# Kernel optimization log

Measured on AMD Instinct MI355X. Metric: run time of the kernel, lower is better.

Reference implementation:

```python
import jax, jax.numpy as jnp
import numpy as np

EPS = 1e-6

def _rmsnorm(x, w):
    var = jnp.mean(x * x, axis=-1, keepdims=True)
    return x * jax.lax.rsqrt(var + EPS) * w

def _act_quant(x):
    # per-token int8 absmax quantization (BitNet b1.58)
    scale = 127.0 / jnp.clip(jnp.max(jnp.abs(x), axis=-1, keepdims=True), 1e-5)
    return jnp.round(jnp.clip(x * scale, -128.0, 127.0)) / scale

def _weight_quant(w):
    # per-tensor ternary quantization with mean-abs scale
    scale = 1.0 / jnp.clip(jnp.mean(jnp.abs(w)), 1e-5)
    return jnp.round(jnp.clip(w * scale, -1.0, 1.0)) / scale

def _ste(x, qfn):
    return x + jax.lax.stop_gradient(qfn(x) - x)

def _bitlinear(x, w):
    xq = _ste(x, _act_quant)
    wq = _ste(w, _weight_quant)
    return jnp.einsum('bsh,fh->bsf', xq, wq)

def setup_inputs() -> dict:
    key = jax.random.key(0)
    k1, k2, k3 = jax.random.split(key, 3)
    B, S, H, F = 4, 4096, 1024, 4096
    x = jax.random.normal(k1, (B, S, H), dtype=jnp.float32)
    norm_w = jnp.ones((H,), dtype=jnp.float32)
    w_up = jax.random.normal(k2, (F, H), dtype=jnp.float32) * (H ** -0.5)
    w_down = jax.random.normal(k3, (H, F), dtype=jnp.float32) * (F ** -0.5)
    return {"x": x, "norm_w": norm_w, "w_up": w_up, "w_down": w_down}

def reference(x, norm_w, w_up, w_down):
    residual = x
    h = _rmsnorm(x, norm_w)
    h = _bitlinear(h, w_up)          # [B,S,F]
    h = jnp.square(jax.nn.relu(h))   # relu^2
    h = _bitlinear(h, w_down)        # [B,S,H]
    return h + residual
```

## Files before the change

kernel.cpp:

```cpp
#include <hip/hip_runtime.h>
#include <hip/hip_fp16.h>

#define M_TOK 16384
#define H_DIM 1024
#define F_DIM 4096

typedef __attribute__((ext_vector_type(4))) int int4v;

static const size_t OFF_H2    = 0;
static const size_t OFF_Q2    = OFF_H2   + 134217728ULL;
static const size_t OFF_XQ    = OFF_Q2   + 67108864ULL;
static const size_t OFF_WQU   = OFF_XQ   + 16777216ULL;
static const size_t OFF_WQD   = OFF_WQU  + 4194304ULL;
static const size_t OFF_DQX   = OFF_WQD  + 4194304ULL;
static const size_t OFF_DQ2   = OFF_DQX  + 65536ULL;
static const size_t OFF_PMAX  = OFF_DQ2  + 65536ULL;
static const size_t OFF_WPART = OFF_PMAX + 4194304ULL;
static const size_t OFF_WSC   = OFF_WPART+ 8192ULL;
static const size_t WS_NEEDED = OFF_WSC  + 16ULL;

__device__ __forceinline__ void ldg_lds16(const void* g, void* l) {
  __builtin_amdgcn_global_load_lds(
      (const __attribute__((address_space(1))) void*)g,
      (__attribute__((address_space(3))) void*)l, 16, 0, 0);
}

__global__ __launch_bounds__(256) void k_wabs(const float* __restrict__ wu,
                                              const float* __restrict__ wd,
                                              float* __restrict__ part) {
  const int b = blockIdx.x;
  const float* w = (b < 1024) ? wu : wd;
  const int cb = b & 1023;
  const size_t base = (size_t)cb * 4096 + threadIdx.x * 4;
  float s = 0.0f;
#pragma unroll
  for (int it = 0; it < 4; ++it) {
    const float4 v = *(const float4*)(w + base + it * 1024);
    s += fabsf(v.x) + fabsf(v.y) + fabsf(v.z) + fabsf(v.w);
  }
#pragma unroll
  for (int sh = 32; sh; sh >>= 1) s += __shfl_xor(s, sh, 64);
  __shared__ float red[4];
  if ((threadIdx.x & 63) == 0) red[threadIdx.x >> 6] = s;
  __syncthreads();
  if (threadIdx.x == 0) part[b] = red[0] + red[1] + red[2] + red[3];
}

__global__ __launch_bounds__(256) void k_wscale(const float* __restrict__ part,
                                                float* __restrict__ wsc) {
  const int b = blockIdx.x;
  const float* p = part + b * 1024;
  float s = p[threadIdx.x] + p[threadIdx.x + 256] + p[threadIdx.x + 512] + p[threadIdx.x + 768];
#pragma unroll
  for (int sh = 32; sh; sh >>= 1) s += __shfl_xor(s, sh, 64);
  __shared__ float red[4];
  if ((threadIdx.x & 63) == 0) red[threadIdx.x >> 6] = s;
  __syncthreads();
  if (threadIdx.x == 0) {
    const float mean = (red[0] + red[1] + red[2] + red[3]) * (1.0f / 4194304.0f);
    const float c = fmaxf(mean, 1e-5f);
    wsc[b * 2]     = c;
    wsc[b * 2 + 1] = 1.0f / c;
  }
}

__global__ __launch_bounds__(256) void k_wquant(const float* __restrict__ wu,
                                                const float* __restrict__ wd,
                                                char* __restrict__ qu,
                                                char* __restrict__ qd,
                                                const float* __restrict__ wsc) {
  const size_t t = (size_t)blockIdx.x * 256 + threadIdx.x;
  const float* w; char* q; float scale; size_t i;
  if (t < 1048576) { w = wu; q = qu; scale = wsc[1]; i = t * 4; }
  else             { w = wd; q = qd; scale = wsc[3]; i = (t - 1048576) * 4; }
  const float4 v = *(const float4*)(w + i);
  const int a = (int)rintf(fminf(fmaxf(v.x * scale, -1.0f), 1.0f));
  const int b = (int)rintf(fminf(fmaxf(v.y * scale, -1.0f), 1.0f));
  const int c = (int)rintf(fminf(fmaxf(v.z * scale, -1.0f), 1.0f));
  const int d = (int)rintf(fminf(fmaxf(v.w * scale, -1.0f), 1.0f));
  *(unsigned*)(q + i) = (a & 255) | ((b & 255) << 8) | ((c & 255) << 16) | ((d & 255) << 24);
}

__global__ __launch_bounds__(256) void k_rmsnorm_quant(const float* __restrict__ x,
                                                       const float* __restrict__ nw,
                                                       char* __restrict__ xq,
                                                       float* __restrict__ dqx) {
  const int row = blockIdx.x;
  const int t = threadIdx.x;
  const float4 v = *(const float4*)(x + (size_t)row * H_DIM + t * 4);
  float ss = v.x * v.x + v.y * v.y + v.z * v.z + v.w * v.w;
#pragma unroll
  for (int sh = 32; sh; sh >>= 1) ss += __shfl_xor(ss, sh, 64);
  __shared__ float red[4];
  __shared__ float redm[4];
  if ((t & 63) == 0) red[t >> 6] = ss;
  __syncthreads();
  ss = red[0] + red[1] + red[2] + red[3];
  const float rinv = 1.0f / sqrtf(ss * (1.0f / 1024.0f) + 1e-6f);
  const float4 w4 = *(const float4*)(nw + t * 4);
  float4 n;
  n.x = v.x * rinv * w4.x;  n.y = v.y * rinv * w4.y;
  n.z = v.z * rinv * w4.z;  n.w = v.w * rinv * w4.w;
  float am = fmaxf(fmaxf(fabsf(n.x), fabsf(n.y)), fmaxf(fabsf(n.z), fabsf(n.w)));
#pragma unroll
  for (int sh = 32; sh; sh >>= 1) am = fmaxf(am, __shfl_xor(am, sh, 64));
  if ((t & 63) == 0) redm[t >> 6] = am;
  __syncthreads();
  am = fmaxf(fmaxf(redm[0], redm[1]), fmaxf(redm[2], redm[3]));
  am = fmaxf(am, 1e-5f);
  const float scale = 127.0f / am;
  const int qa = (int)rintf(fminf(fmaxf(n.x * scale, -128.0f), 127.0f));
  const int qb = (int)rintf(fminf(fmaxf(n.y * scale, -128.0f), 127.0f));
  const int qc = (int)rintf(fminf(fmaxf(n.z * scale, -128.0f), 127.0f));
  const int qd = (int)rintf(fminf(fmaxf(n.w * scale, -128.0f), 127.0f));
  *(unsigned*)(xq + (size_t)row * H_DIM + t * 4) =
      (qa & 255) | ((qb & 255) << 8) | ((qc & 255) << 16) | ((qd & 255) << 24);
  if (t == 0) dqx[row] = am * (1.0f / 127.0f);
}

template <int LDA_, int LDB_, int KTILES>
__device__ __forceinline__ void gemm_core(const char* __restrict__ A,
                                          const char* __restrict__ B,
                                          int mBase, int nBase,
                                          char* As, char* Bs, int4v acc[4][4]) {
  const int t = threadIdx.x;
  const int lane = t & 63;
  const int wm = (t >> 6) & 1;
  const int wn = t >> 7;
  const int sRow = t >> 3;
  const int sSeg = (t & 7) ^ (sRow & 7);
  const char* Ag = A + (size_t)(mBase + sRow) * LDA_ + sSeg * 16;
  const char* Bg = B + (size_t)(nBase + sRow) * LDB_ + sSeg * 16;
  char* Al = As + t * 16;
  char* Bl = Bs + t * 16;
  const int q = lane >> 4;
  const int rA = wm * 64 + (lane & 15);
  const int rB = wn * 64 + (lane & 15);
  const int swA = rA & 7;
  const int swB = rB & 7;

  for (int kt = 0; kt < KTILES; ++kt) {
    __syncthreads();
#pragma unroll
    for (int n = 0; n < 4; ++n) ldg_lds16(Ag + (size_t)n * 32 * LDA_, Al + n * 4096);
#pragma unroll
    for (int n = 0; n < 4; ++n) ldg_lds16(Bg + (size_t)n * 32 * LDB_, Bl + n * 4096);
    Ag += 128; Bg += 128;
    __syncthreads();
#pragma unroll
    for (int ks = 0; ks < 2; ++ks) {
      const int ao = (((ks * 4 + q) ^ swA) << 4);
      const int bo = (((ks * 4 + q) ^ swB) << 4);
      int4v a[4], b[4];
#pragma unroll
      for (int i = 0; i < 4; ++i) a[i] = *(const int4v*)(As + (rA + i * 16) * 128 + ao);
#pragma unroll
      for (int j = 0; j < 4; ++j) b[j] = *(const int4v*)(Bs + (rB + j * 16) * 128 + bo);
#pragma unroll
      for (int i = 0; i < 4; ++i)
#pragma unroll
        for (int j = 0; j < 4; ++j)
          acc[i][j] = __builtin_amdgcn_mfma_i32_16x16x64_i8(a[i], b[j], acc[i][j], 0, 0, 0);
    }
  }
}

__global__ __launch_bounds__(256, 2) void k_gemm1(const char* __restrict__ xq,
                                                  const char* __restrict__ wq,
                                                  const float* __restrict__ wsc,
                                                  const float* __restrict__ dqx,
                                                  __half* __restrict__ h2,
                                                  float* __restrict__ pmax) {
  __shared__ char smem[32768];
  int4v acc[4][4];
#pragma unroll
  for (int i = 0; i < 4; ++i)
#pragma unroll
    for (int j = 0; j < 4; ++j) acc[i][j] = (int4v){0, 0, 0, 0};
  const int mBase = blockIdx.x * 128;
  const int nBase = blockIdx.y * 128;
  gemm_core<H_DIM, H_DIM, 8>(xq, wq, mBase, nBase, smem, smem + 16384, acc);

  const int t = threadIdx.x;
  const int lane = t & 63;
  const int wm = (t >> 6) & 1;
  const int wn = t >> 7;
  const float dqw = wsc[0];
#pragma unroll
  for (int i = 0; i < 4; ++i) {
    const int rbase = mBase + wm * 64 + i * 16 + ((lane >> 4) << 2);
    const float4 dq4 = *(const float4*)(dqx + rbase);
    const float* dqp = (const float*)&dq4;
    float rmax[4] = {0.0f, 0.0f, 0.0f, 0.0f};
#pragma unroll
    for (int j = 0; j < 4; ++j) {
      const int col = nBase + wn * 64 + j * 16 + (lane & 15);
#pragma unroll
      for (int r = 0; r < 4; ++r) {
        float v = (float)acc[i][j][r] * dqp[r] * dqw;
        v = fmaxf(v, 0.0f);
        v = v * v;
        const __half h = __float2half(v);
        h2[(size_t)(rbase + r) * F_DIM + col] = h;
        rmax[r] = fmaxf(rmax[r], __half2float(h));
      }
    }
#pragma unroll
    for (int s = 1; s < 16; s <<= 1) {
#pragma unroll
      for (int r = 0; r < 4; ++r) rmax[r] = fmaxf(rmax[r], __shfl_xor(rmax[r], s, 64));
    }
    if ((lane & 15) == 0) {
      const int nb2 = blockIdx.y * 2 + wn;
#pragma unroll
      for (int r = 0; r < 4; ++r) pmax[(size_t)nb2 * M_TOK + rbase + r] = rmax[r];
    }
  }
}

__global__ __launch_bounds__(256) void k_quant2(const __half* __restrict__ h2,
                                                const float* __restrict__ pmax,
                                                char* __restrict__ q2,
                                                float* __restrict__ dq2) {
  const int row = blockIdx.x;
  const int t = threadIdx.x;
  __shared__ float sm;
  if (t < 64) {
    float m = pmax[(size_t)t * M_TOK + row];
#pragma unroll
    for (int sh = 32; sh; sh >>= 1) m = fmaxf(m, __shfl_xor(m, sh, 64));
    if (t == 0) sm = fmaxf(m, 1e-5f);
  }
  __syncthreads();
  const float mx = sm;
  const float s = 127.0f / mx;
  if (t == 0) dq2[row] = mx * (1.0f / 127.0f);
  const size_t i = (size_t)row * F_DIM + t * 16;
  __half2 hh[8];
  *(float4*)(hh)     = *(const float4*)(h2 + i);
  *(float4*)(hh + 4) = *(const float4*)(h2 + i + 8);
  unsigned u[4];
#pragma unroll
  for (int k = 0; k < 4; ++k) {
    const int q0 = (int)rintf(fminf(__low2float(hh[2 * k]) * s, 127.0f));
    const int q1 = (int)rintf(fminf(__high2float(hh[2 * k]) * s, 127.0f));
    const int q2i = (int)rintf(fminf(__low2float(hh[2 * k + 1]) * s, 127.0f));
    const int q3 = (int)rintf(fminf(__high2float(hh[2 * k + 1]) * s, 127.0f));
    u[k] = (q0 & 255) | ((q1 & 255) << 8) | ((q2i & 255) << 16) | ((q3 & 255) << 24);
  }
  *(uint4*)(q2 + i) = make_uint4(u[0], u[1], u[2], u[3]);
}

__global__ __launch_bounds__(256, 2) void k_gemm2(const char* __restrict__ q2,
                                                  const char* __restrict__ wq,
                                                  const float* __restrict__ wsc,
                                                  const float* __restrict__ dq2,
                                                  const float* __restrict__ x,
                                                  float* __restrict__ out) {
  __shared__ char smem[32768];
  int4v acc[4][4];
#pragma unroll
  for (int i = 0; i < 4; ++i)
#pragma unroll
    for (int j = 0; j < 4; ++j) acc[i][j] = (int4v){0, 0, 0, 0};
  const int mBase = blockIdx.x * 128;
  const int nBase = blockIdx.y * 128;
  gemm_core<F_DIM, F_DIM, 32>(q2, wq, mBase, nBase, smem, smem + 16384, acc);

  const int t = threadIdx.x;
  const int lane = t & 63;
  const int wm = (t >> 6) & 1;
  const int wn = t >> 7;
  const float dqw = wsc[2];
#pragma unroll
  for (int i = 0; i < 4; ++i) {
    const int rbase = mBase + wm * 64 + i * 16 + ((lane >> 4) << 2);
    const float4 dq4 = *(const float4*)(dq2 + rbase);
    const float* dqp = (const float*)&dq4;
#pragma unroll
    for (int j = 0; j < 4; ++j) {
      const int col = nBase + wn * 64 + j * 16 + (lane & 15);
#pragma unroll
      for (int r = 0; r < 4; ++r) {
        const size_t idx = (size_t)(rbase + r) * H_DIM + col;
        out[idx] = (float)acc[i][j][r] * dqp[r] * dqw + x[idx];
      }
    }
  }
}

extern "C" void kernel_launch(void* const* d_in, const int* in_sizes, int n_in,
                              void* d_out, int out_size, void* d_ws, size_t ws_size,
                              hipStream_t stream) {
  const float* x  = (const float*)d_in[0];
  const float* nw = (const float*)d_in[1];
  const float* wu = (const float*)d_in[2];
  const float* wd = (const float*)d_in[3];
  float* out = (float*)d_out;
  char* ws = (char*)d_ws;
  if (ws_size < WS_NEEDED) return;

  __half* h2     = (__half*)(ws + OFF_H2);
  char* q2       = ws + OFF_Q2;
  char* xq       = ws + OFF_XQ;
  char* wqu      = ws + OFF_WQU;
  char* wqd      = ws + OFF_WQD;
  float* dqx     = (float*)(ws + OFF_DQX);
  float* dq2     = (float*)(ws + OFF_DQ2);
  float* pmax    = (float*)(ws + OFF_PMAX);
  float* wpart   = (float*)(ws + OFF_WPART);
  float* wsc     = (float*)(ws + OFF_WSC);

  k_wabs<<<2048, 256, 0, stream>>>(wu, wd, wpart);
  k_wscale<<<2, 256, 0, stream>>>(wpart, wsc);
  k_wquant<<<8192, 256, 0, stream>>>(wu, wd, wqu, wqd, wsc);
  k_rmsnorm_quant<<<M_TOK, 256, 0, stream>>>(x, nw, xq, dqx);
  k_gemm1<<<dim3(M_TOK / 128, F_DIM / 128), 256, 0, stream>>>(xq, wqu, wsc, dqx, h2, pmax);
  k_quant2<<<M_TOK, 256, 0, stream>>>(h2, pmax, q2, dq2);
  k_gemm2<<<dim3(M_TOK / 128, H_DIM / 128), 256, 0, stream>>>(q2, wqd, wsc, dq2, x, out);
}
```

Measured before the change: 363.3 us.

## Double-buffer LDS tiles in int8 GEMM core to overlap loads with MFMA

Turns the shared GEMM main loop into a two-stage ping-pong pipeline. The next K-tile is issued as a global-to-LDS load into the alternate buffer while MFMAs run on the current one, so each iteration needs one barrier instead of two. It also raises wave priority around the MFMA block with s_setprio. LDS per block doubles to 64 KB, which could limit occupancy relative to the launch_bounds target of 2 blocks per CU.

Result: slower. 385.6 us (+6.1%).

```diff
diff --git a/kernel.cpp b/kernel.cpp
--- a/kernel.cpp
+++ b/kernel.cpp
@@ -122,7 +122,7 @@
 __device__ __forceinline__ void gemm_core(const char* __restrict__ A,
                                           const char* __restrict__ B,
                                           int mBase, int nBase,
-                                          char* As, char* Bs, int4v acc[4][4]) {
+                                          char* __restrict__ smem, int4v acc[4][4]) {
   const int t = threadIdx.x;
   const int lane = t & 63;
   const int wm = (t >> 6) & 1;
@@ -131,37 +131,54 @@
   const int sSeg = (t & 7) ^ (sRow & 7);
   const char* Ag = A + (size_t)(mBase + sRow) * LDA_ + sSeg * 16;
   const char* Bg = B + (size_t)(nBase + sRow) * LDB_ + sSeg * 16;
-  char* Al = As + t * 16;
-  char* Bl = Bs + t * 16;
   const int q = lane >> 4;
   const int rA = wm * 64 + (lane & 15);
   const int rB = wn * 64 + (lane & 15);
   const int swA = rA & 7;
   const int swB = rB & 7;
 
+#pragma unroll
+  for (int n = 0; n < 4; ++n)
+    ldg_lds16(Ag + (size_t)n * 32 * LDA_, smem + t * 16 + n * 4096);
+#pragma unroll
+  for (int n = 0; n < 4; ++n)
+    ldg_lds16(Bg + (size_t)n * 32 * LDB_, smem + 16384 + t * 16 + n * 4096);
+  Ag += 128; Bg += 128;
+  __syncthreads();
+
+  int curOff = 0;
   for (int kt = 0; kt < KTILES; ++kt) {
-    __syncthreads();
-#pragma unroll
-    for (int n = 0; n < 4; ++n) ldg_lds16(Ag + (size_t)n * 32 * LDA_, Al + n * 4096);
-#pragma unroll
-    for (int n = 0; n < 4; ++n) ldg_lds16(Bg + (size_t)n * 32 * LDB_, Bl + n * 4096);
-    Ag += 128; Bg += 128;
-    __syncthreads();
+    const int nxtOff = curOff ^ 32768;
+    if (kt + 1 < KTILES) {
+#pragma unroll
+      for (int n = 0; n < 4; ++n)
+        ldg_lds16(Ag + (size_t)n * 32 * LDA_, smem + nxtOff + t * 16 + n * 4096);
+#pragma unroll
+      for (int n = 0; n < 4; ++n)
+        ldg_lds16(Bg + (size_t)n * 32 * LDB_, smem + nxtOff + 16384 + t * 16 + n * 4096);
+      Ag += 128; Bg += 128;
+    }
+    const char* Asb = smem + curOff;
+    const char* Bsb = smem + curOff + 16384;
 #pragma unroll
     for (int ks = 0; ks < 2; ++ks) {
       const int ao = (((ks * 4 + q) ^ swA) << 4);
       const int bo = (((ks * 4 + q) ^ swB) << 4);
       int4v a[4], b[4];
 #pragma unroll
-      for (int i = 0; i < 4; ++i) a[i] = *(const int4v*)(As + (rA + i * 16) * 128 + ao);
-#pragma unroll
-      for (int j = 0; j < 4; ++j) b[j] = *(const int4v*)(Bs + (rB + j * 16) * 128 + bo);
+      for (int i = 0; i < 4; ++i) a[i] = *(const int4v*)(Asb + (rA + i * 16) * 128 + ao);
+#pragma unroll
+      for (int j = 0; j < 4; ++j) b[j] = *(const int4v*)(Bsb + (rB + j * 16) * 128 + bo);
+      __builtin_amdgcn_s_setprio(1);
 #pragma unroll
       for (int i = 0; i < 4; ++i)
 #pragma unroll
         for (int j = 0; j < 4; ++j)
           acc[i][j] = __builtin_amdgcn_mfma_i32_16x16x64_i8(a[i], b[j], acc[i][j], 0, 0, 0);
-    }
+      __builtin_amdgcn_s_setprio(0);
+    }
+    __syncthreads();
+    curOff = nxtOff;
   }
 }
 
@@ -171,7 +188,7 @@
                                                   const float* __restrict__ dqx,
                                                   __half* __restrict__ h2,
                                                   float* __restrict__ pmax) {
-  __shared__ char smem[32768];
+  __shared__ char smem[65536];
   int4v acc[4][4];
 #pragma unroll
   for (int i = 0; i < 4; ++i)
@@ -179,7 +196,7 @@
     for (int j = 0; j < 4; ++j) acc[i][j] = (int4v){0, 0, 0, 0};
   const int mBase = blockIdx.x * 128;
   const int nBase = blockIdx.y * 128;
-  gemm_core<H_DIM, H_DIM, 8>(xq, wq, mBase, nBase, smem, smem + 16384, acc);
+  gemm_core<H_DIM, H_DIM, 8>(xq, wq, mBase, nBase, smem, acc);
 
   const int t = threadIdx.x;
   const int lane = t & 63;
@@ -257,7 +274,7 @@
                                                   const float* __restrict__ dq2,
                                                   const float* __restrict__ x,
                                                   float* __restrict__ out) {
-  __shared__ char smem[32768];
+  __shared__ char smem[65536];
   int4v acc[4][4];
 #pragma unroll
   for (int i = 0; i < 4; ++i)
@@ -265,7 +282,7 @@
     for (int j = 0; j < 4; ++j) acc[i][j] = (int4v){0, 0, 0, 0};
   const int mBase = blockIdx.x * 128;
   const int nBase = blockIdx.y * 128;
-  gemm_core<F_DIM, F_DIM, 32>(q2, wq, mBase, nBase, smem, smem + 16384, acc);
+  gemm_core<F_DIM, F_DIM, 32>(q2, wq, mBase, nBase, smem, acc);
 
   const int t = threadIdx.x;
   const int lane = t & 63;
```

## Use 256x256 int8 GEMM tiles with double-buffered LDS prefetch

Applied to the files above, without the earlier changes.

Both int8 MFMA GEMMs move from 128x128 tiles with 256 threads to 256x256 tiles with 512 threads. Each wave now holds an 8x4 accumulator block. The k-loop double-buffers LDS and issues the next tile's global-to-LDS loads while it computes on the current one. It also raises wave priority around MFMA bursts with s_setprio. The aim is to hide global load latency and raise operand reuse per byte loaded. The cost is a 128 KB LDS footprint and more registers, which limits occupancy to one block per CU, and gemm2 launches only 256 blocks.

After: 340.3 us. 1.07x faster.

```diff
diff --git a/kernel.cpp b/kernel.cpp
--- a/kernel.cpp
+++ b/kernel.cpp
@@ -118,83 +118,113 @@
   if (t == 0) dqx[row] = am * (1.0f / 127.0f);
 }
 
-template <int LDA_, int LDB_, int KTILES>
-__device__ __forceinline__ void gemm_core(const char* __restrict__ A,
-                                          const char* __restrict__ B,
-                                          int mBase, int nBase,
-                                          char* As, char* Bs, int4v acc[4][4]) {
+template <int LD>
+__device__ __forceinline__ void stage4(const char* g, char* l) {
+  ldg_lds16(g,                     l);
+  ldg_lds16(g + (size_t)64  * LD,  l + 8192);
+  ldg_lds16(g + (size_t)128 * LD,  l + 16384);
+  ldg_lds16(g + (size_t)192 * LD,  l + 24576);
+}
+
+template <int LDA_, int LDB_, int KT>
+__device__ __forceinline__ void gemm_core256(const char* __restrict__ A,
+                                             const char* __restrict__ B,
+                                             int mBase, int nBase,
+                                             char* __restrict__ smem,
+                                             int4v acc[8][4]) {
   const int t = threadIdx.x;
   const int lane = t & 63;
-  const int wm = (t >> 6) & 1;
-  const int wn = t >> 7;
+  const int w = t >> 6;
+  const int wm = w & 1;
+  const int wn = w >> 1;
   const int sRow = t >> 3;
   const int sSeg = (t & 7) ^ (sRow & 7);
   const char* Ag = A + (size_t)(mBase + sRow) * LDA_ + sSeg * 16;
   const char* Bg = B + (size_t)(nBase + sRow) * LDB_ + sSeg * 16;
-  char* Al = As + t * 16;
-  char* Bl = Bs + t * 16;
-  const int q = lane >> 4;
-  const int rA = wm * 64 + (lane & 15);
-  const int rB = wn * 64 + (lane & 15);
-  const int swA = rA & 7;
-  const int swB = rB & 7;
-
-  for (int kt = 0; kt < KTILES; ++kt) {
+  const int q  = lane >> 4;
+  const int fr = lane & 15;
+  const int sw = fr & 7;
+
+  stage4<LDA_>(Ag, smem + (t << 4));
+  stage4<LDB_>(Bg, smem + 32768 + (t << 4));
+  __syncthreads();
+
+  int cur = 0;
+  for (int kt = 0; kt < KT; ++kt) {
+    const int nxt = cur ^ 65536;
+    const char* Ab = smem + cur + wm * 16384;
+    const char* Bb = smem + cur + 32768 + wn * 8192;
+    int4v a[8], b[4];
+    if (kt + 1 < KT) stage4<LDA_>(Ag + (size_t)(kt + 1) * 128, smem + nxt + (t << 4));
+    {
+      const int ao = ((q ^ sw) << 4);
+#pragma unroll
+      for (int i = 0; i < 8; ++i) a[i] = *(const int4v*)(Ab + (i * 16 + fr) * 128 + ao);
+#pragma unroll
+      for (int j = 0; j < 4; ++j) b[j] = *(const int4v*)(Bb + (j * 16 + fr) * 128 + ao);
+    }
+    __builtin_amdgcn_s_barrier();
+    __builtin_amdgcn_s_setprio(1);
+#pragma unroll
+    for (int i = 0; i < 8; ++i)
+#pragma unroll
+      for (int j = 0; j < 4; ++j)
+        acc[i][j] = __builtin_amdgcn_mfma_i32_16x16x64_i8(a[i], b[j], acc[i][j], 0, 0, 0);
+    __builtin_amdgcn_s_setprio(0);
+    if (kt + 1 < KT) stage4<LDB_>(Bg + (size_t)(kt + 1) * 128, smem + nxt + 32768 + (t << 4));
+    {
+      const int ao = (((4 + q) ^ sw) << 4);
+#pragma unroll
+      for (int i = 0; i < 8; ++i) a[i] = *(const int4v*)(Ab + (i * 16 + fr) * 128 + ao);
+#pragma unroll
+      for (int j = 0; j < 4; ++j) b[j] = *(const int4v*)(Bb + (j * 16 + fr) * 128 + ao);
+    }
+    __builtin_amdgcn_s_barrier();
+    __builtin_amdgcn_s_setprio(1);
+#pragma unroll
+    for (int i = 0; i < 8; ++i)
+#pragma unroll
+      for (int j = 0; j < 4; ++j)
+        acc[i][j] = __builtin_amdgcn_mfma_i32_16x16x64_i8(a[i], b[j], acc[i][j], 0, 0, 0);
+    __builtin_amdgcn_s_setprio(0);
     __syncthreads();
-#pragma unroll
-    for (int n = 0; n < 4; ++n) ldg_lds16(Ag + (size_t)n * 32 * LDA_, Al + n * 4096);
-#pragma unroll
-    for (int n = 0; n < 4; ++n) ldg_lds16(Bg + (size_t)n * 32 * LDB_, Bl + n * 4096);
-    Ag += 128; Bg += 128;
-    __syncthreads();
-#pragma unroll
-    for (int ks = 0; ks < 2; ++ks) {
-      const int ao = (((ks * 4 + q) ^ swA) << 4);
-      const int bo = (((ks * 4 + q) ^ swB) << 4);
-      int4v a[4], b[4];
-#pragma unroll
-      for (int i = 0; i < 4; ++i) a[i] = *(const int4v*)(As + (rA + i * 16) * 128 + ao);
-#pragma unroll
-      for (int j = 0; j < 4; ++j) b[j] = *(const int4v*)(Bs + (rB + j * 16) * 128 + bo);
-#pragma unroll
-      for (int i = 0; i < 4; ++i)
-#pragma unroll
-        for (int j = 0; j < 4; ++j)
-          acc[i][j] = __builtin_amdgcn_mfma_i32_16x16x64_i8(a[i], b[j], acc[i][j], 0, 0, 0);
-    }
-  }
-}
-
-__global__ __launch_bounds__(256, 2) void k_gemm1(const char* __restrict__ xq,
+    cur = nxt;
+  }
+}
+
+__global__ __launch_bounds__(512, 2) void k_gemm1(const char* __restrict__ xq,
                                                   const char* __restrict__ wq,
                                                   const float* __restrict__ wsc,
                                                   const float* __restrict__ dqx,
                                                   __half* __restrict__ h2,
                                                   float* __restrict__ pmax) {
-  __shared__ char smem[32768];
-  int4v acc[4][4];
-#pragma unroll
-  for (int i = 0; i < 4; ++i)
+  __shared__ char smem[131072];
+  int4v acc[8][4];
+#pragma unroll
+  for (int i = 0; i < 8; ++i)
 #pragma unroll
     for (int j = 0; j < 4; ++j) acc[i][j] = (int4v){0, 0, 0, 0};
-  const int mBase = blockIdx.x * 128;
-  const int nBase = blockIdx.y * 128;
-  gemm_core<H_DIM, H_DIM, 8>(xq, wq, mBase, nBase, smem, smem + 16384, acc);
+  const int mBase = blockIdx.x * 256;
+  const int nBase = blockIdx.y * 256;
+  gemm_core256<H_DIM, H_DIM, 8>(xq, wq, mBase, nBase, smem, acc);
 
   const int t = threadIdx.x;
   const int lane = t & 63;
-  const int wm = (t >> 6) & 1;
-  const int wn = t >> 7;
+  const int w = t >> 6;
+  const int wm = w & 1;
+  const int wn = w >> 1;
+  const int q  = lane >> 4;
+  const int fr = lane & 15;
   const float dqw = wsc[0];
 #pragma unroll
-  for (int i = 0; i < 4; ++i) {
-    const int rbase = mBase + wm * 64 + i * 16 + ((lane >> 4) << 2);
+  for (int i = 0; i < 8; ++i) {
+    const int rbase = mBase + wm * 128 + i * 16 + (q << 2);
     const float4 dq4 = *(const float4*)(dqx + rbase);
     const float* dqp = (const float*)&dq4;
     float rmax[4] = {0.0f, 0.0f, 0.0f, 0.0f};
 #pragma unroll
     for (int j = 0; j < 4; ++j) {
-      const int col = nBase + wn * 64 + j * 16 + (lane & 15);
+      const int col = nBase + wn * 64 + j * 16 + fr;
 #pragma unroll
       for (int r = 0; r < 4; ++r) {
         float v = (float)acc[i][j][r] * dqp[r] * dqw;
@@ -210,8 +240,8 @@
 #pragma unroll
       for (int r = 0; r < 4; ++r) rmax[r] = fmaxf(rmax[r], __shfl_xor(rmax[r], s, 64));
     }
-    if ((lane & 15) == 0) {
-      const int nb2 = blockIdx.y * 2 + wn;
+    if (fr == 0) {
+      const int nb2 = blockIdx.y * 4 + wn;
 #pragma unroll
       for (int r = 0; r < 4; ++r) pmax[(size_t)nb2 * M_TOK + rbase + r] = rmax[r];
     }
@@ -251,35 +281,38 @@
   *(uint4*)(q2 + i) = make_uint4(u[0], u[1], u[2], u[3]);
 }
 
-__global__ __launch_bounds__(256, 2) void k_gemm2(const char* __restrict__ q2,
+__global__ __launch_bounds__(512, 2) void k_gemm2(const char* __restrict__ q2,
                                                   const char* __restrict__ wq,
                                                   const float* __restrict__ wsc,
                                                   const float* __restrict__ dq2,
                                                   const float* __restrict__ x,
                                                   float* __restrict__ out) {
-  __shared__ char smem[32768];
-  int4v acc[4][4];
-#pragma unroll
-  for (int i = 0; i < 4; ++i)
+  __shared__ char smem[131072];
+  int4v acc[8][4];
+#pragma unroll
+  for (int i = 0; i < 8; ++i)
 #pragma unroll
     for (int j = 0; j < 4; ++j) acc[i][j] = (int4v){0, 0, 0, 0};
-  const int mBase = blockIdx.x * 128;
-  const int nBase = blockIdx.y * 128;
-  gemm_core<F_DIM, F_DIM, 32>(q2, wq, mBase, nBase, smem, smem + 16384, acc);
+  const int mBase = blockIdx.x * 256;
+  const int nBase = blockIdx.y * 256;
+  gemm_core256<F_DIM, F_DIM, 32>(q2, wq, mBase, nBase, smem, acc);
 
   const int t = threadIdx.x;
   const int lane = t & 63;
-  const int wm = (t >> 6) & 1;
-  const int wn = t >> 7;
+  const int w = t >> 6;
+  const int wm = w & 1;
+  const int wn = w >> 1;
+  const int q  = lane >> 4;
+  const int fr = lane & 15;
   const float dqw = wsc[2];
 #pragma unroll
-  for (int i = 0; i < 4; ++i) {
-    const int rbase = mBase + wm * 64 + i * 16 + ((lane >> 4) << 2);
+  for (int i = 0; i < 8; ++i) {
+    const int rbase = mBase + wm * 128 + i * 16 + (q << 2);
     const float4 dq4 = *(const float4*)(dq2 + rbase);
     const float* dqp = (const float*)&dq4;
 #pragma unroll
     for (int j = 0; j < 4; ++j) {
-      const int col = nBase + wn * 64 + j * 16 + (lane & 15);
+      const int col = nBase + wn * 64 + j * 16 + fr;
 #pragma unroll
       for (int r = 0; r < 4; ++r) {
         const size_t idx = (size_t)(rbase + r) * H_DIM + col;
@@ -315,7 +348,7 @@
   k_wscale<<<2, 256, 0, stream>>>(wpart, wsc);
   k_wquant<<<8192, 256, 0, stream>>>(wu, wd, wqu, wqd, wsc);
   k_rmsnorm_quant<<<M_TOK, 256, 0, stream>>>(x, nw, xq, dqx);
-  k_gemm1<<<dim3(M_TOK / 128, F_DIM / 128), 256, 0, stream>>>(xq, wqu, wsc, dqx, h2, pmax);
+  k_gemm1<<<dim3(M_TOK / 256, F_DIM / 256), 512, 0, stream>>>(xq, wqu, wsc, dqx, h2, pmax);
   k_quant2<<<M_TOK, 256, 0, stream>>>(h2, pmax, q2, dq2);
-  k_gemm2<<<dim3(M_TOK / 128, H_DIM / 128), 256, 0, stream>>>(q2, wqd, wsc, dq2, x, out);
-}
+  k_gemm2<<<dim3(M_TOK / 256, H_DIM / 256), 512, 0, stream>>>(q2, wqd, wsc, dq2, x, out);
+}
```
